# Kernel tuning notes

Measured on AMD Instinct MI355X. Metric: run time of the kernel, lower is better.

Reference implementation:

```python
import jax, jax.numpy as jnp
import numpy as np

H = 1024
B = 64
S = 1024
V = 50257
L = 3  # GRU layers


def setup_inputs() -> dict:
    key = jax.random.key(0)
    ks = jax.random.split(key, 12)
    sc = 0.02
    return {
        "input_seq": jax.random.randint(ks[0], (B,), 0, V),
        "last_hidden": jax.random.normal(ks[1], (L, B, H), jnp.float32) * sc,
        "encoder_outputs": jax.random.normal(ks[2], (S, B, H), jnp.float32) * sc,
        "emb_table": jax.random.normal(ks[3], (V, H), jnp.float32) * sc,
        "w_ih": jax.random.normal(ks[4], (L, 3 * H, H), jnp.float32) * sc,
        "w_hh": jax.random.normal(ks[5], (L, 3 * H, H), jnp.float32) * sc,
        "b_ih": jax.random.normal(ks[6], (L, 3 * H), jnp.float32) * sc,
        "b_hh": jax.random.normal(ks[7], (L, 3 * H), jnp.float32) * sc,
        "concat_w": jax.random.normal(ks[8], (H, 2 * H), jnp.float32) * sc,
        "concat_b": jax.random.normal(ks[9], (H,), jnp.float32) * sc,
        "out_w": jax.random.normal(ks[10], (V, H), jnp.float32) * sc,
        "out_b": jax.random.normal(ks[11], (V,), jnp.float32) * sc,
    }


def _gru_step(x, h, w_ih, w_hh, b_ih, b_hh):
    # x, h: [B, H]; weights per PyTorch GRU layout (r, z, n gates stacked)
    gi = x @ w_ih.T + b_ih  # [B, 3H]
    gh = h @ w_hh.T + b_hh  # [B, 3H]
    i_r, i_z, i_n = jnp.split(gi, 3, axis=-1)
    h_r, h_z, h_n = jnp.split(gh, 3, axis=-1)
    r = jax.nn.sigmoid(i_r + h_r)
    z = jax.nn.sigmoid(i_z + h_z)
    n = jnp.tanh(i_n + r * h_n)
    return (1.0 - z) * n + z * h


def reference(input_seq, last_hidden, encoder_outputs, emb_table,
              w_ih, w_hh, b_ih, b_hh, concat_w, concat_b, out_w, out_b):
    # Embed current token (decoder uses its own embedding of size hidden_dim).
    x = emb_table[input_seq]  # [B, H]; dropout is identity at eval time
    # 3-layer GRU, single time step.
    new_h = []
    for l in range(L):
        h_l = _gru_step(x, last_hidden[l], w_ih[l], w_hh[l], b_ih[l], b_hh[l])
        new_h.append(h_l)
        x = h_l  # inter-layer dropout is identity at eval time
    hidden = jnp.stack(new_h, axis=0)  # [L, B, H]
    rnn_output = x  # [B, H] (top layer output, seq len 1)
    # Dot attention: score(b, s) = <rnn_output[b], encoder_outputs[s, b]>
    scores = jnp.einsum('bh,sbh->bs', rnn_output, encoder_outputs)  # [B, S]
    attn = jax.nn.softmax(scores, axis=-1)  # [B, S]
    attn_weights = attn[:, None, :]  # [B, 1, S]
    context = jnp.einsum('bs,sbh->bh', attn, encoder_outputs)  # [B, H]
    concat_input = jnp.concatenate([rnn_output, context], axis=-1)  # [B, 2H]
    concat_output = jnp.tanh(concat_input @ concat_w.T + concat_b)  # [B, H]
    output = concat_output @ out_w.T + out_b  # [B, V]
    return (output, hidden, attn_weights)
```

## Files before the change

### kernel.cpp

```cpp
#include <hip/hip_runtime.h>
#include <hip/hip_bf16.h>
#include <float.h>

#define B_ 64
#define H_ 1024
#define S_ 1024
#define V_ 50257
#define L_ 3
#define G3H 3072
#define N_GATES 6144
#define NT_K 16
#define KSPL_GRU 8
#define KSPL_CAT 16

typedef __attribute__((ext_vector_type(8))) short short8v;
typedef __attribute__((ext_vector_type(4))) float f32x4;

__device__ __forceinline__ ushort rnd_bf16(float x) {
    uint u = __float_as_uint(x);
    return (ushort)((u + 0x7fffu + ((u >> 16) & 1u)) >> 16);
}

__device__ __forceinline__ void split_bf16(float x, ushort& hi, ushort& lo) {
    uint u = __float_as_uint(x);
    uint h = u & 0xffff0000u;
    hi = (ushort)(h >> 16);
    float r = x - __uint_as_float(h);
    uint ur = __float_as_uint(r);
    lo = (ushort)((ur + 0x7fffu + ((ur >> 16) & 1u)) >> 16);
}

__global__ __launch_bounds__(256) void gemm_bf16_lds(
    const float* __restrict__ A0, const int* __restrict__ seq,
    const float* __restrict__ A1, int lda,
    const float* __restrict__ W0, const float* __restrict__ W1, int ldw,
    int Nhalf, float* __restrict__ Cpart, int N, int K) {
    __shared__ ushort AhL[2][64 * 64];
    __shared__ ushort AlL[2][64 * 64];
    __shared__ ushort WtL[2][64 * 64];

    int tid = threadIdx.x;
    int w = tid >> 6, l = tid & 63;
    int lr = l & 15;
    int lk = l >> 4;

    int n0 = blockIdx.x * 64;
    const float* A = A0;
    const float* W = W0;
    const int* sq = seq;
    int ncol0 = n0;
    if (n0 >= Nhalf) { A = A1; W = W1; ncol0 = n0 - Nhalf; sq = nullptr; }

    int srow = tid >> 2;
    int sqk = tid & 3;
    const float* Asrc = A + (size_t)(sq ? sq[srow] : srow) * lda;
    const float* Wsrc = W + (size_t)(ncol0 + srow) * ldw;

    int kChunk = K / gridDim.y;
    int kBeg = blockIdx.y * kChunk;
    int nt = kChunk >> 6;

    union SV { short8v v; ushort u[8]; };

    float4 rA[4], rW[4];
    auto load_regs = [&](int kt) {
        int kb = kBeg + kt * 64 + sqk * 16;
#pragma unroll
        for (int i = 0; i < 4; i++) {
            rA[i] = *(const float4*)&Asrc[kb + i * 4];
            rW[i] = *(const float4*)&Wsrc[kb + i * 4];
        }
    };
    auto write_lds = [&](int buf) {
        int s0 = (2 * sqk) ^ (srow & 7);
        int s1 = (2 * sqk + 1) ^ (srow & 7);
        int base = srow * 64;
        SV h0, h1, l0, l1, q0, q1;
        const float* fa = (const float*)&rA[0];
        const float* fw = (const float*)&rW[0];
#pragma unroll
        for (int j = 0; j < 8; j++) {
            split_bf16(fa[j], h0.u[j], l0.u[j]);
            split_bf16(fa[8 + j], h1.u[j], l1.u[j]);
            q0.u[j] = rnd_bf16(fw[j]);
            q1.u[j] = rnd_bf16(fw[8 + j]);
        }
        *(short8v*)&AhL[buf][base + s0 * 8] = h0.v;
        *(short8v*)&AhL[buf][base + s1 * 8] = h1.v;
        *(short8v*)&AlL[buf][base + s0 * 8] = l0.v;
        *(short8v*)&AlL[buf][base + s1 * 8] = l1.v;
        *(short8v*)&WtL[buf][base + s0 * 8] = q0.v;
        *(short8v*)&WtL[buf][base + s1 * 8] = q1.v;
    };

    f32x4 acc[4];
#pragma unroll
    for (int mt = 0; mt < 4; mt++) acc[mt] = (f32x4){0.f, 0.f, 0.f, 0.f};

    load_regs(0);
    write_lds(0);
    __syncthreads();

    int wrow = w * 16 + lr;
    for (int kt = 0; kt < nt; kt++) {
        if (kt + 1 < nt) load_regs(kt + 1);

        int cur = kt & 1;
#pragma unroll
        for (int ks = 0; ks < 2; ks++) {
            int slot = ks * 4 + lk;
            short8v wf = *(const short8v*)&WtL[cur][wrow * 64 + ((slot ^ (wrow & 7)) << 3)];
#pragma unroll
            for (int mt = 0; mt < 4; mt++) {
                int arow = mt * 16 + lr;
                int so = (slot ^ (arow & 7)) << 3;
                short8v ah = *(const short8v*)&AhL[cur][arow * 64 + so];
                short8v al = *(const short8v*)&AlL[cur][arow * 64 + so];
                acc[mt] = __builtin_amdgcn_mfma_f32_16x16x32_bf16(ah, wf, acc[mt], 0, 0, 0);
                acc[mt] = __builtin_amdgcn_mfma_f32_16x16x32_bf16(al, wf, acc[mt], 0, 0, 0);
            }
        }

        if (kt + 1 < nt) {
            write_lds((kt + 1) & 1);
            __syncthreads();
        }
    }

    float* Pp = Cpart + (size_t)blockIdx.y * 64 * N;
    int col = n0 + wrow;
#pragma unroll
    for (int mt = 0; mt < 4; mt++) {
#pragma unroll
        for (int r = 0; r < 4; r++) {
            int row = mt * 16 + lk * 4 + r;
            Pp[(size_t)row * N + col] = acc[mt][r];
        }
    }
}

__global__ __launch_bounds__(256) void gru_combine_k(
    const float* __restrict__ P, const float* __restrict__ b_ih,
    const float* __restrict__ b_hh, const float* __restrict__ hprev,
    float* __restrict__ hout) {
    int idx = blockIdx.x * 256 + threadIdx.x;
    int b = idx >> 10, j = idx & 1023;
    const size_t stride = (size_t)64 * N_GATES;
    const float* rowp = P + (size_t)b * N_GATES;

    float ir = 0.f, iz = 0.f, in_ = 0.f, hr = 0.f, hz = 0.f, hn = 0.f;
#pragma unroll
    for (int kc = 0; kc < KSPL_GRU; kc++) {
        const float* p = rowp + kc * stride;
        ir += p[j];        iz += p[j + 1024];        in_ += p[j + 2048];
        hr += p[3072 + j]; hz += p[3072 + j + 1024]; hn += p[3072 + j + 2048];
    }
    ir += b_ih[j]; iz += b_ih[j + 1024]; in_ += b_ih[j + 2048];
    hr += b_hh[j]; hz += b_hh[j + 1024]; hn += b_hh[j + 2048];

    float r = 1.f / (1.f + __expf(-(ir + hr)));
    float z = 1.f / (1.f + __expf(-(iz + hz)));
    float n = tanhf(in_ + r * hn);
    float hp = hprev[idx];
    hout[idx] = (1.f - z) * n + z * hp;
}

__global__ __launch_bounds__(256) void attn_pass1(
    const float* __restrict__ rnn, const float* __restrict__ enc,
    float* __restrict__ scores, float* __restrict__ ctxPart,
    float* __restrict__ chunkMax) {
    __shared__ float lm[4];
    __shared__ float lc[4][1024];

    int bid = blockIdx.x;
    int b = bid >> 4, scv = bid & 15;
    int tid = threadIdx.x;
    int w = tid >> 6, lane = tid & 63;

    const float4* rr = (const float4*)(rnn + (size_t)b * H_);
    float4 r0 = rr[0 * 64 + lane], r1 = rr[1 * 64 + lane];
    float4 r2 = rr[2 * 64 + lane], r3 = rr[3 * 64 + lane];

    float m = -FLT_MAX;
    float4 c0 = {0, 0, 0, 0}, c1 = {0, 0, 0, 0}, c2 = {0, 0, 0, 0}, c3 = {0, 0, 0, 0};

    int s0 = scv * 64 + w * 16;
    for (int si = 0; si < 16; si++) {
        int s = s0 + si;
        const float4* er = (const float4*)(enc + ((size_t)s * B_ + b) * H_);
        float4 e0 = er[0 * 64 + lane], e1 = er[1 * 64 + lane];
        float4 e2 = er[2 * 64 + lane], e3 = er[3 * 64 + lane];

        float d = e0.x * r0.x + e0.y * r0.y + e0.z * r0.z + e0.w * r0.w;
        d += e1.x * r1.x + e1.y * r1.y + e1.z * r1.z + e1.w * r1.w;
        d += e2.x * r2.x + e2.y * r2.y + e2.z * r2.z + e2.w * r2.w;
        d += e3.x * r3.x + e3.y * r3.y + e3.z * r3.z + e3.w * r3.w;
#pragma unroll
        for (int off = 32; off; off >>= 1) d += __shfl_xor(d, off, 64);
        if (lane == 0) scores[(size_t)b * S_ + s] = d;

        if (d > m) {
            float scale = __expf(m - d);
            c0.x *= scale; c0.y *= scale; c0.z *= scale; c0.w *= scale;
            c1.x *= scale; c1.y *= scale; c1.z *= scale; c1.w *= scale;
            c2.x *= scale; c2.y *= scale; c2.z *= scale; c2.w *= scale;
            c3.x *= scale; c3.y *= scale; c3.z *= scale; c3.w *= scale;
            m = d;
        }
        float p = __expf(d - m);
        c0.x += p * e0.x; c0.y += p * e0.y; c0.z += p * e0.z; c0.w += p * e0.w;
        c1.x += p * e1.x; c1.y += p * e1.y; c1.z += p * e1.z; c1.w += p * e1.w;
        c2.x += p * e2.x; c2.y += p * e2.y; c2.z += p * e2.z; c2.w += p * e2.w;
        c3.x += p * e3.x; c3.y += p * e3.y; c3.z += p * e3.z; c3.w += p * e3.w;
    }

    if (lane == 0) lm[w] = m;
    __syncthreads();
    float M = fmaxf(fmaxf(lm[0], lm[1]), fmaxf(lm[2], lm[3]));
    float sw = __expf(m - M);
    float4* lw = (float4*)&lc[w][0];
    float4 t;
    t.x = c0.x * sw; t.y = c0.y * sw; t.z = c0.z * sw; t.w = c0.w * sw; lw[0 * 64 + lane] = t;
    t.x = c1.x * sw; t.y = c1.y * sw; t.z = c1.z * sw; t.w = c1.w * sw; lw[1 * 64 + lane] = t;
    t.x = c2.x * sw; t.y = c2.y * sw; t.z = c2.z * sw; t.w = c2.w * sw; lw[2 * 64 + lane] = t;
    t.x = c3.x * sw; t.y = c3.y * sw; t.z = c3.z * sw; t.w = c3.w * sw; lw[3 * 64 + lane] = t;
    __syncthreads();

    float4 s4 = *(const float4*)&lc[0][tid * 4];
    float4 a1 = *(const float4*)&lc[1][tid * 4];
    float4 a2 = *(const float4*)&lc[2][tid * 4];
    float4 a3 = *(const float4*)&lc[3][tid * 4];
    s4.x += a1.x + a2.x + a3.x; s4.y += a1.y + a2.y + a3.y;
    s4.z += a1.z + a2.z + a3.z; s4.w += a1.w + a2.w + a3.w;
    *(float4*)&ctxPart[(size_t)bid * H_ + tid * 4] = s4;
    if (tid == 0) chunkMax[bid] = M;
}

__global__ __launch_bounds__(256) void attn_pass2(
    const float* __restrict__ scores, const float* __restrict__ chunkMax,
    const float* __restrict__ ctxPart, const float* __restrict__ rnn,
    float* __restrict__ attn, float* __restrict__ concat_in) {
    __shared__ float red[256];
    int b = blockIdx.x, tid = threadIdx.x;

    float v[4];
#pragma unroll
    for (int q = 0; q < 4; q++) v[q] = scores[(size_t)b * S_ + q * 256 + tid];
    float mx = fmaxf(fmaxf(v[0], v[1]), fmaxf(v[2], v[3]));
    red[tid] = mx; __syncthreads();
    for (int s = 128; s; s >>= 1) {
        if (tid < s) red[tid] = fmaxf(red[tid], red[tid + s]);
        __syncthreads();
    }
    float M = red[0]; __syncthreads();
    float e[4], sum = 0.f;
#pragma unroll
    for (int q = 0; q < 4; q++) { e[q] = __expf(v[q] - M); sum += e[q]; }
    red[tid] = sum; __syncthreads();
    for (int s = 128; s; s >>= 1) {
        if (tid < s) red[tid] += red[tid + s];
        __syncthreads();
    }
    float inv = 1.f / red[0];
#pragma unroll
    for (int q = 0; q < 4; q++) attn[(size_t)b * S_ + q * 256 + tid] = e[q] * inv;

    float4 acc = {0, 0, 0, 0};
#pragma unroll
    for (int c = 0; c < 16; c++) {
        float scl = __expf(chunkMax[b * 16 + c] - M);
        float4 part = *(const float4*)&ctxPart[((size_t)b * 16 + c) * H_ + tid * 4];
        acc.x += scl * part.x; acc.y += scl * part.y;
        acc.z += scl * part.z; acc.w += scl * part.w;
    }
    acc.x *= inv; acc.y *= inv; acc.z *= inv; acc.w *= inv;
    *(float4*)&concat_in[(size_t)b * 2048 + 1024 + tid * 4] = acc;
    *(float4*)&concat_in[(size_t)b * 2048 + tid * 4] =
        *(const float4*)&rnn[(size_t)b * H_ + tid * 4];
}

__global__ __launch_bounds__(256) void concat_combine_k(const float* __restrict__ P,
                                                        const float* __restrict__ bias,
                                                        ushort* __restrict__ Ahi,
                                                        ushort* __restrict__ Alo) {
    int idx = blockIdx.x * 256 + threadIdx.x;
    int b = idx >> 10, h = idx & 1023;
    float s = 0.f;
#pragma unroll
    for (int kc = 0; kc < KSPL_CAT; kc++) s += P[(size_t)kc * 65536 + (size_t)b * H_ + h];
    float v = tanhf(s + bias[h]);
    ushort hi, lo;
    split_bf16(v, hi, lo);
    Ahi[idx] = hi;
    Alo[idx] = lo;
}

__global__ __launch_bounds__(256) void gemm_out_bf16(
    const ushort* __restrict__ Ahi, const ushort* __restrict__ Alo,
    const float* __restrict__ W, const float* __restrict__ bias,
    float* __restrict__ out) {
    __shared__ ushort AhL[2][64 * 64];
    __shared__ ushort AlL[2][64 * 64];
    __shared__ ushort WtL[2][64 * 64];

    int tid = threadIdx.x;
    int w = tid >> 6, l = tid & 63;
    int lr = l & 15;
    int lk = l >> 4;

    int n0 = blockIdx.x * 64;

    int srow = tid >> 2;
    int sqk = tid & 3;
    int wrow_g = n0 + srow;
    const float* Wsrc = W + (size_t)(wrow_g < V_ ? wrow_g : 0) * H_;

    union SV { short8v v; ushort u[8]; };

    short8v rAh0, rAh1, rAl0, rAl1;
    float4 rW[4];

    auto load_regs = [&](int kt) {
        int kb = kt * 64 + sqk * 16;
        rAh0 = *(const short8v*)&Ahi[(size_t)srow * H_ + kb];
        rAh1 = *(const short8v*)&Ahi[(size_t)srow * H_ + kb + 8];
        rAl0 = *(const short8v*)&Alo[(size_t)srow * H_ + kb];
        rAl1 = *(const short8v*)&Alo[(size_t)srow * H_ + kb + 8];
#pragma unroll
        for (int i = 0; i < 4; i++) rW[i] = *(const float4*)&Wsrc[kb + i * 4];
    };

    auto write_lds = [&](int buf) {
        int s0 = (2 * sqk) ^ (srow & 7);
        int s1 = (2 * sqk + 1) ^ (srow & 7);
        int base = srow * 64;
        *(short8v*)&AhL[buf][base + s0 * 8] = rAh0;
        *(short8v*)&AhL[buf][base + s1 * 8] = rAh1;
        *(short8v*)&AlL[buf][base + s0 * 8] = rAl0;
        *(short8v*)&AlL[buf][base + s1 * 8] = rAl1;
        SV p0, p1;
        const float* f = (const float*)&rW[0];
#pragma unroll
        for (int j = 0; j < 8; j++) {
            p0.u[j] = rnd_bf16(f[j]);
            p1.u[j] = rnd_bf16(f[8 + j]);
        }
        *(short8v*)&WtL[buf][base + s0 * 8] = p0.v;
        *(short8v*)&WtL[buf][base + s1 * 8] = p1.v;
    };

    f32x4 acc[4];
#pragma unroll
    for (int mt = 0; mt < 4; mt++) acc[mt] = (f32x4){0.f, 0.f, 0.f, 0.f};

    load_regs(0);
    write_lds(0);
    __syncthreads();

    int wrow = w * 16 + lr;
    for (int kt = 0; kt < NT_K; kt++) {
        if (kt + 1 < NT_K) load_regs(kt + 1);

        int cur = kt & 1;
#pragma unroll
        for (int ks = 0; ks < 2; ks++) {
            int slot = ks * 4 + lk;
            short8v wf = *(const short8v*)&WtL[cur][wrow * 64 + ((slot ^ (wrow & 7)) << 3)];
#pragma unroll
            for (int mt = 0; mt < 4; mt++) {
                int arow = mt * 16 + lr;
                int so = (slot ^ (arow & 7)) << 3;
                short8v ah = *(const short8v*)&AhL[cur][arow * 64 + so];
                short8v al = *(const short8v*)&AlL[cur][arow * 64 + so];
                acc[mt] = __builtin_amdgcn_mfma_f32_16x16x32_bf16(ah, wf, acc[mt], 0, 0, 0);
                acc[mt] = __builtin_amdgcn_mfma_f32_16x16x32_bf16(al, wf, acc[mt], 0, 0, 0);
            }
        }

        if (kt + 1 < NT_K) {
            write_lds((kt + 1) & 1);
            __syncthreads();
        }
    }

    __syncthreads();
    float* et = (float*)&AhL[0][0];
#pragma unroll
    for (int mt = 0; mt < 4; mt++) {
#pragma unroll
        for (int r = 0; r < 4; r++) {
            int row = mt * 16 + lk * 4 + r;
            et[row * 64 + wrow] = acc[mt][r];
        }
    }
    __syncthreads();

    int col = tid & 63;
    int gc = n0 + col;
    int rg = tid >> 6;
    if (gc < V_) {
        float b = bias[gc];
#pragma unroll
        for (int rr = 0; rr < 16; rr++) {
            int orow = rg * 16 + rr;
            out[(size_t)orow * V_ + gc] = et[orow * 64 + col] + b;
        }
    }
}

extern "C" void kernel_launch(void* const* d_in, const int* in_sizes, int n_in,
                              void* d_out, int out_size, void* d_ws, size_t ws_size,
                              hipStream_t stream) {
    const int* seq = (const int*)d_in[0];
    const float* last_hidden = (const float*)d_in[1];
    const float* enc = (const float*)d_in[2];
    const float* emb = (const float*)d_in[3];
    const float* w_ih = (const float*)d_in[4];
    const float* w_hh = (const float*)d_in[5];
    const float* b_ih = (const float*)d_in[6];
    const float* b_hh = (const float*)d_in[7];
    const float* concat_w = (const float*)d_in[8];
    const float* concat_b = (const float*)d_in[9];
    const float* out_w = (const float*)d_in[10];
    const float* out_b = (const float*)d_in[11];

    float* out = (float*)d_out;
    float* out_hidden = out + (size_t)B_ * V_;
    float* out_attn = out_hidden + (size_t)L_ * B_ * H_;

    float* ws = (float*)d_ws;
    float* gatesP = ws;
    float* scores = gatesP + 3145728;
    float* chunkMax = scores + 65536;
    float* ctxPart = chunkMax + 1024;
    float* concat_in = ctxPart + 1048576;
    float* concatP = concat_in + 131072;
    ushort* Ahi = (ushort*)(concatP + 1048576);
    ushort* Alo = Ahi + 65536;

    for (int l = 0; l < L_; l++) {
        const float* xl = (l == 0) ? emb : out_hidden + (size_t)(l - 1) * B_ * H_;
        const int* sq = (l == 0) ? seq : nullptr;
        const float* hl = last_hidden + (size_t)l * B_ * H_;
        gemm_bf16_lds<<<dim3(N_GATES / 64, KSPL_GRU), 256, 0, stream>>>(
            xl, sq, hl, H_,
            w_ih + (size_t)l * G3H * H_, w_hh + (size_t)l * G3H * H_, H_, G3H,
            gatesP, N_GATES, H_);
        gru_combine_k<<<256, 256, 0, stream>>>(gatesP, b_ih + (size_t)l * G3H,
                                               b_hh + (size_t)l * G3H, hl,
                                               out_hidden + (size_t)l * B_ * H_);
    }
    const float* rnn = out_hidden + (size_t)2 * B_ * H_;

    attn_pass1<<<1024, 256, 0, stream>>>(rnn, enc, scores, ctxPart, chunkMax);
    attn_pass2<<<64, 256, 0, stream>>>(scores, chunkMax, ctxPart, rnn,
                                       out_attn, concat_in);

    gemm_bf16_lds<<<dim3(H_ / 64, KSPL_CAT), 256, 0, stream>>>(
        concat_in, nullptr, concat_in, 2048, concat_w, concat_w, 2048, 1 << 30,
        concatP, H_, 2048);
    concat_combine_k<<<256, 256, 0, stream>>>(concatP, concat_b, Ahi, Alo);

    gemm_out_bf16<<<(V_ + 63) / 64, 256, 0, stream>>>(Ahi, Alo, out_w, out_b, out);
}
```

Before: 184.0 us.

## Split output projection GEMM over K with separate combine kernel, single-buffered LDS

The vocabulary projection GEMM now splits the K dimension in two (grid y=2), writing partial sums to a padded workspace. A new combine kernel adds the two partials and the bias. LDS drops from double-buffering to a single buffer with extra barriers, and the wave-to-tile mapping changes so each wave owns an A row block and loops over weight tiles. This doubles block count for better occupancy across CUs, at the cost of extra global traffic for partials (~26MB) and an extra launch.

New measurement: 188.0 us. 1.02x slower.

```diff
diff --git a/kernel.cpp b/kernel.cpp
--- a/kernel.cpp
+++ b/kernel.cpp
@@ -6,10 +6,10 @@
 #define H_ 1024
 #define S_ 1024
 #define V_ 50257
+#define VPAD 50304
 #define L_ 3
 #define G3H 3072
 #define N_GATES 6144
-#define NT_K 16
 #define KSPL_GRU 8
 #define KSPL_CAT 16
 
@@ -297,11 +297,11 @@
 
 __global__ __launch_bounds__(256) void gemm_out_bf16(
     const ushort* __restrict__ Ahi, const ushort* __restrict__ Alo,
-    const float* __restrict__ W, const float* __restrict__ bias,
-    float* __restrict__ out) {
-    __shared__ ushort AhL[2][64 * 64];
-    __shared__ ushort AlL[2][64 * 64];
-    __shared__ ushort WtL[2][64 * 64];
+    const float* __restrict__ W, float* __restrict__ P) {
+    __shared__ ushort Lds[3 * 64 * 64];
+    ushort* AhL = Lds;
+    ushort* AlL = Lds + 4096;
+    ushort* WtL = Lds + 8192;
 
     int tid = threadIdx.x;
     int w = tid >> 6, l = tid & 63;
@@ -309,6 +309,8 @@
     int lk = l >> 4;
 
     int n0 = blockIdx.x * 64;
+    int ks0 = blockIdx.y;
+    int ktBeg = ks0 * 8;
 
     int srow = tid >> 2;
     int sqk = tid & 3;
@@ -330,14 +332,14 @@
         for (int i = 0; i < 4; i++) rW[i] = *(const float4*)&Wsrc[kb + i * 4];
     };
 
-    auto write_lds = [&](int buf) {
+    auto write_lds = [&]() {
         int s0 = (2 * sqk) ^ (srow & 7);
         int s1 = (2 * sqk + 1) ^ (srow & 7);
         int base = srow * 64;
-        *(short8v*)&AhL[buf][base + s0 * 8] = rAh0;
-        *(short8v*)&AhL[buf][base + s1 * 8] = rAh1;
-        *(short8v*)&AlL[buf][base + s0 * 8] = rAl0;
-        *(short8v*)&AlL[buf][base + s1 * 8] = rAl1;
+        *(short8v*)&AhL[base + s0 * 8] = rAh0;
+        *(short8v*)&AhL[base + s1 * 8] = rAh1;
+        *(short8v*)&AlL[base + s0 * 8] = rAl0;
+        *(short8v*)&AlL[base + s1 * 8] = rAl1;
         SV p0, p1;
         const float* f = (const float*)&rW[0];
 #pragma unroll
@@ -345,66 +347,75 @@
             p0.u[j] = rnd_bf16(f[j]);
             p1.u[j] = rnd_bf16(f[8 + j]);
         }
-        *(short8v*)&WtL[buf][base + s0 * 8] = p0.v;
-        *(short8v*)&WtL[buf][base + s1 * 8] = p1.v;
+        *(short8v*)&WtL[base + s0 * 8] = p0.v;
+        *(short8v*)&WtL[base + s1 * 8] = p1.v;
     };
 
     f32x4 acc[4];
 #pragma unroll
-    for (int mt = 0; mt < 4; mt++) acc[mt] = (f32x4){0.f, 0.f, 0.f, 0.f};
-
-    load_regs(0);
-    write_lds(0);
+    for (int nt = 0; nt < 4; nt++) acc[nt] = (f32x4){0.f, 0.f, 0.f, 0.f};
+
+    load_regs(ktBeg);
+    write_lds();
     __syncthreads();
 
-    int wrow = w * 16 + lr;
-    for (int kt = 0; kt < NT_K; kt++) {
-        if (kt + 1 < NT_K) load_regs(kt + 1);
-
-        int cur = kt & 1;
+    int arow = w * 16 + lr;
+    int abase = arow * 64;
+    int amask = (arow & 7);
+
+    for (int kt = 0; kt < 8; kt++) {
+        if (kt + 1 < 8) load_regs(ktBeg + kt + 1);
+
 #pragma unroll
         for (int ks = 0; ks < 2; ks++) {
             int slot = ks * 4 + lk;
-            short8v wf = *(const short8v*)&WtL[cur][wrow * 64 + ((slot ^ (wrow & 7)) << 3)];
-#pragma unroll
-            for (int mt = 0; mt < 4; mt++) {
-                int arow = mt * 16 + lr;
-                int so = (slot ^ (arow & 7)) << 3;
-                short8v ah = *(const short8v*)&AhL[cur][arow * 64 + so];
-                short8v al = *(const short8v*)&AlL[cur][arow * 64 + so];
-                acc[mt] = __builtin_amdgcn_mfma_f32_16x16x32_bf16(ah, wf, acc[mt], 0, 0, 0);
-                acc[mt] = __builtin_amdgcn_mfma_f32_16x16x32_bf16(al, wf, acc[mt], 0, 0, 0);
+            short8v ah = *(const short8v*)&AhL[abase + ((slot ^ amask) << 3)];
+            short8v al = *(const short8v*)&AlL[abase + ((slot ^ amask) << 3)];
+#pragma unroll
+            for (int nt = 0; nt < 4; nt++) {
+                int wrow = nt * 16 + lr;
+                short8v wf = *(const short8v*)&WtL[wrow * 64 + ((slot ^ (wrow & 7)) << 3)];
+                acc[nt] = __builtin_amdgcn_mfma_f32_16x16x32_bf16(ah, wf, acc[nt], 0, 0, 0);
+                acc[nt] = __builtin_amdgcn_mfma_f32_16x16x32_bf16(al, wf, acc[nt], 0, 0, 0);
             }
         }
 
-        if (kt + 1 < NT_K) {
-            write_lds((kt + 1) & 1);
+        __syncthreads();
+        if (kt + 1 < 8) {
+            write_lds();
             __syncthreads();
         }
     }
 
+    float* et = (float*)Lds;
+#pragma unroll
+    for (int nt = 0; nt < 4; nt++) {
+#pragma unroll
+        for (int r = 0; r < 4; r++) {
+            int row = w * 16 + lk * 4 + r;
+            et[row * 64 + nt * 16 + lr] = acc[nt][r];
+        }
+    }
     __syncthreads();
-    float* et = (float*)&AhL[0][0];
-#pragma unroll
-    for (int mt = 0; mt < 4; mt++) {
-#pragma unroll
-        for (int r = 0; r < 4; r++) {
-            int row = mt * 16 + lk * 4 + r;
-            et[row * 64 + wrow] = acc[mt][r];
-        }
-    }
-    __syncthreads();
-
+
+    float* Pp = P + (size_t)ks0 * 64 * VPAD;
     int col = tid & 63;
-    int gc = n0 + col;
     int rg = tid >> 6;
-    if (gc < V_) {
-        float b = bias[gc];
-#pragma unroll
-        for (int rr = 0; rr < 16; rr++) {
-            int orow = rg * 16 + rr;
-            out[(size_t)orow * V_ + gc] = et[orow * 64 + col] + b;
-        }
+#pragma unroll
+    for (int rr = 0; rr < 16; rr++) {
+        int row = rg * 16 + rr;
+        Pp[(size_t)row * VPAD + n0 + col] = et[row * 64 + col];
+    }
+}
+
+__global__ __launch_bounds__(256) void out_combine_k(const float* __restrict__ P,
+                                                     const float* __restrict__ bias,
+                                                     float* __restrict__ out) {
+    int n = blockIdx.x * 256 + threadIdx.x;
+    int b = blockIdx.y;
+    if (n < V_) {
+        out[(size_t)b * V_ + n] = P[(size_t)b * VPAD + n] +
+                                  P[((size_t)64 + b) * VPAD + n] + bias[n];
     }
 }
 
@@ -437,6 +448,7 @@
     float* concatP = concat_in + 131072;
     ushort* Ahi = (ushort*)(concatP + 1048576);
     ushort* Alo = Ahi + 65536;
+    float* outP = (float*)(Alo + 65536);
 
     for (int l = 0; l < L_; l++) {
         const float* xl = (l == 0) ? emb : out_hidden + (size_t)(l - 1) * B_ * H_;
@@ -461,5 +473,6 @@
         concatP, H_, 2048);
     concat_combine_k<<<256, 256, 0, stream>>>(concatP, concat_b, Ahi, Alo);
 
-    gemm_out_bf16<<<(V_ + 63) / 64, 256, 0, stream>>>(Ahi, Alo, out_w, out_b, out);
-}
+    gemm_out_bf16<<<dim3(VPAD / 64, 2), 256, 0, stream>>>(Ahi, Alo, out_w, outP);
+    out_combine_k<<<dim3((V_ + 255) / 256, 64), 256, 0, stream>>>(outP, out_b, out);
+}
```

## Shrink output GEMM tile to 32 columns and read activations directly from global

Applied to the files above, without the earlier changes.

The vocabulary projection kernel now handles 32 output columns per block instead of 64, doubling the grid to about 1572 blocks. The bf16 hi/lo activation fragments are loaded straight from global (L2-resident) into registers rather than staged in LDS, so only the weight tile is double-buffered in LDS. This cuts LDS footprint and per-block latency and raises occupancy for a kernel bound by streaming fp32 weights, at the cost of redundant global reads of the small activation matrix by every wave.

New measurement: 193.2 us. +5.0%, slower.

```diff
diff --git a/kernel.cpp b/kernel.cpp
--- a/kernel.cpp
+++ b/kernel.cpp
@@ -6,10 +6,10 @@
 #define H_ 1024
 #define S_ 1024
 #define V_ 50257
+#define VPAD 50304
 #define L_ 3
 #define G3H 3072
 #define N_GATES 6144
-#define NT_K 16
 #define KSPL_GRU 8
 #define KSPL_CAT 16
 
@@ -299,111 +299,97 @@
     const ushort* __restrict__ Ahi, const ushort* __restrict__ Alo,
     const float* __restrict__ W, const float* __restrict__ bias,
     float* __restrict__ out) {
-    __shared__ ushort AhL[2][64 * 64];
-    __shared__ ushort AlL[2][64 * 64];
-    __shared__ ushort WtL[2][64 * 64];
+    __shared__ ushort WtL[2][32 * 64];
 
     int tid = threadIdx.x;
     int w = tid >> 6, l = tid & 63;
     int lr = l & 15;
     int lk = l >> 4;
 
-    int n0 = blockIdx.x * 64;
-
-    int srow = tid >> 2;
-    int sqk = tid & 3;
-    int wrow_g = n0 + srow;
-    const float* Wsrc = W + (size_t)(wrow_g < V_ ? wrow_g : 0) * H_;
+    int n0 = blockIdx.x * 32;
+
+    int srow = tid >> 3;
+    int sqk = tid & 7;
+    int wrg = n0 + srow;
+    const float* Wsrc = W + (size_t)(wrg < V_ ? wrg : 0) * H_;
 
     union SV { short8v v; ushort u[8]; };
 
-    short8v rAh0, rAh1, rAl0, rAl1;
-    float4 rW[4];
-
-    auto load_regs = [&](int kt) {
-        int kb = kt * 64 + sqk * 16;
-        rAh0 = *(const short8v*)&Ahi[(size_t)srow * H_ + kb];
-        rAh1 = *(const short8v*)&Ahi[(size_t)srow * H_ + kb + 8];
-        rAl0 = *(const short8v*)&Alo[(size_t)srow * H_ + kb];
-        rAl1 = *(const short8v*)&Alo[(size_t)srow * H_ + kb + 8];
-#pragma unroll
-        for (int i = 0; i < 4; i++) rW[i] = *(const float4*)&Wsrc[kb + i * 4];
+    float4 rW0, rW1;
+    auto load_wregs = [&](int kt) {
+        int kb = kt * 64 + sqk * 8;
+        rW0 = *(const float4*)&Wsrc[kb];
+        rW1 = *(const float4*)&Wsrc[kb + 4];
     };
-
     auto write_lds = [&](int buf) {
-        int s0 = (2 * sqk) ^ (srow & 7);
-        int s1 = (2 * sqk + 1) ^ (srow & 7);
-        int base = srow * 64;
-        *(short8v*)&AhL[buf][base + s0 * 8] = rAh0;
-        *(short8v*)&AhL[buf][base + s1 * 8] = rAh1;
-        *(short8v*)&AlL[buf][base + s0 * 8] = rAl0;
-        *(short8v*)&AlL[buf][base + s1 * 8] = rAl1;
-        SV p0, p1;
-        const float* f = (const float*)&rW[0];
-#pragma unroll
-        for (int j = 0; j < 8; j++) {
-            p0.u[j] = rnd_bf16(f[j]);
-            p1.u[j] = rnd_bf16(f[8 + j]);
-        }
-        *(short8v*)&WtL[buf][base + s0 * 8] = p0.v;
-        *(short8v*)&WtL[buf][base + s1 * 8] = p1.v;
+        int s = sqk ^ (srow & 7);
+        SV p;
+        const float* f0 = (const float*)&rW0;
+        const float* f1 = (const float*)&rW1;
+#pragma unroll
+        for (int j = 0; j < 4; j++) {
+            p.u[j] = rnd_bf16(f0[j]);
+            p.u[j + 4] = rnd_bf16(f1[j]);
+        }
+        *(short8v*)&WtL[buf][srow * 64 + s * 8] = p.v;
     };
 
-    f32x4 acc[4];
-#pragma unroll
-    for (int mt = 0; mt < 4; mt++) acc[mt] = (f32x4){0.f, 0.f, 0.f, 0.f};
-
-    load_regs(0);
+    f32x4 acc[2];
+    acc[0] = (f32x4){0.f, 0.f, 0.f, 0.f};
+    acc[1] = (f32x4){0.f, 0.f, 0.f, 0.f};
+
+    load_wregs(0);
     write_lds(0);
     __syncthreads();
 
-    int wrow = w * 16 + lr;
-    for (int kt = 0; kt < NT_K; kt++) {
-        if (kt + 1 < NT_K) load_regs(kt + 1);
+    const ushort* Ah = Ahi + (size_t)(w * 16 + lr) * H_;
+    const ushort* Al = Alo + (size_t)(w * 16 + lr) * H_;
+
+    for (int kt = 0; kt < 16; kt++) {
+        if (kt + 1 < 16) load_wregs(kt + 1);
+
+        int kb = kt * 64 + lk * 8;
+        short8v ah0 = *(const short8v*)&Ah[kb];
+        short8v al0 = *(const short8v*)&Al[kb];
+        short8v ah1 = *(const short8v*)&Ah[kb + 32];
+        short8v al1 = *(const short8v*)&Al[kb + 32];
 
         int cur = kt & 1;
 #pragma unroll
-        for (int ks = 0; ks < 2; ks++) {
-            int slot = ks * 4 + lk;
-            short8v wf = *(const short8v*)&WtL[cur][wrow * 64 + ((slot ^ (wrow & 7)) << 3)];
-#pragma unroll
-            for (int mt = 0; mt < 4; mt++) {
-                int arow = mt * 16 + lr;
-                int so = (slot ^ (arow & 7)) << 3;
-                short8v ah = *(const short8v*)&AhL[cur][arow * 64 + so];
-                short8v al = *(const short8v*)&AlL[cur][arow * 64 + so];
-                acc[mt] = __builtin_amdgcn_mfma_f32_16x16x32_bf16(ah, wf, acc[mt], 0, 0, 0);
-                acc[mt] = __builtin_amdgcn_mfma_f32_16x16x32_bf16(al, wf, acc[mt], 0, 0, 0);
-            }
-        }
-
-        if (kt + 1 < NT_K) {
-            write_lds((kt + 1) & 1);
-            __syncthreads();
-        }
-    }
-
+        for (int nt = 0; nt < 2; nt++) {
+            int wr = nt * 16 + lr;
+            short8v wf0 = *(const short8v*)&WtL[cur][wr * 64 + ((lk ^ (wr & 7)) << 3)];
+            short8v wf1 = *(const short8v*)&WtL[cur][wr * 64 + (((4 + lk) ^ (wr & 7)) << 3)];
+            acc[nt] = __builtin_amdgcn_mfma_f32_16x16x32_bf16(ah0, wf0, acc[nt], 0, 0, 0);
+            acc[nt] = __builtin_amdgcn_mfma_f32_16x16x32_bf16(al0, wf0, acc[nt], 0, 0, 0);
+            acc[nt] = __builtin_amdgcn_mfma_f32_16x16x32_bf16(ah1, wf1, acc[nt], 0, 0, 0);
+            acc[nt] = __builtin_amdgcn_mfma_f32_16x16x32_bf16(al1, wf1, acc[nt], 0, 0, 0);
+        }
+
+        if (kt + 1 < 16) write_lds(cur ^ 1);
+        __syncthreads();
+    }
+
+    float* et = (float*)&WtL[0][0];
+#pragma unroll
+    for (int nt = 0; nt < 2; nt++) {
+#pragma unroll
+        for (int r = 0; r < 4; r++) {
+            int row = w * 16 + lk * 4 + r;
+            et[row * 32 + nt * 16 + lr] = acc[nt][r];
+        }
+    }
     __syncthreads();
-    float* et = (float*)&AhL[0][0];
-#pragma unroll
-    for (int mt = 0; mt < 4; mt++) {
-#pragma unroll
-        for (int r = 0; r < 4; r++) {
-            int row = mt * 16 + lk * 4 + r;
-            et[row * 64 + wrow] = acc[mt][r];
-        }
-    }
-    __syncthreads();
-
-    int col = tid & 63;
+
+    int col = tid & 31;
+    int rg = tid >> 5;
     int gc = n0 + col;
-    int rg = tid >> 6;
     if (gc < V_) {
         float b = bias[gc];
 #pragma unroll
-        for (int rr = 0; rr < 16; rr++) {
-            int orow = rg * 16 + rr;
-            out[(size_t)orow * V_ + gc] = et[orow * 64 + col] + b;
+        for (int rr = 0; rr < 8; rr++) {
+            int row = rg * 8 + rr;
+            out[(size_t)row * V_ + gc] = et[row * 32 + col] + b;
         }
     }
 }
@@ -461,5 +447,5 @@
         concatP, H_, 2048);
     concat_combine_k<<<256, 256, 0, stream>>>(concatP, concat_b, Ahi, Alo);
 
-    gemm_out_bf16<<<(V_ + 63) / 64, 256, 0, stream>>>(Ahi, Alo, out_w, out_b, out);
-}
+    gemm_out_bf16<<<VPAD / 32, 256, 0, stream>>>(Ahi, Alo, out_w, out_b, out);
+}
```
